# Performance work log

Hardware: AMD Instinct MI355X
Metric: run time of the kernel (lower is better)

## Reference

```python
import jax, jax.numpy as jnp
import numpy as np
import math

TOPK = 13
NC = 80
ALPHA = 1.0
BETA = 6.0
EPS = 1e-9


def _xyxy2wh(b):
    return b[..., 2:4] - b[..., 0:2]


def _bbox_ciou(box1, box2, eps=1e-7):
    # box1: [bs,nmax,1,4] gt, box2: [bs,1,na,4] pred, xyxy. Returns [bs,nmax,na].
    b1x1, b1y1, b1x2, b1y2 = jnp.split(box1, 4, axis=-1)
    b2x1, b2y1, b2x2, b2y2 = jnp.split(box2, 4, axis=-1)
    w1, h1 = b1x2 - b1x1, b1y2 - b1y1 + eps
    w2, h2 = b2x2 - b2x1, b2y2 - b2y1 + eps
    inter = jnp.clip(jnp.minimum(b1x2, b2x2) - jnp.maximum(b1x1, b2x1), 0) * \
            jnp.clip(jnp.minimum(b1y2, b2y2) - jnp.maximum(b1y1, b2y1), 0)
    union = w1 * h1 + w2 * h2 - inter + eps
    iou = inter / union
    cw = jnp.maximum(b1x2, b2x2) - jnp.minimum(b1x1, b2x1)  # enclosing box
    ch = jnp.maximum(b1y2, b2y2) - jnp.minimum(b1y1, b2y1)
    c2 = cw ** 2 + ch ** 2 + eps
    rho2 = ((b2x1 + b2x2 - b1x1 - b1x2) ** 2 + (b2y1 + b2y2 - b1y1 - b1y2) ** 2) / 4.0
    v = (4.0 / math.pi ** 2) * (jnp.arctan(w2 / h2) - jnp.arctan(w1 / h1)) ** 2
    a = jax.lax.stop_gradient(v / (v - iou + (1.0 + eps)))  # torch.no_grad alpha
    return (iou - (rho2 / c2 + v * a))[..., 0]


def tal_forward(pd_scores, pd_bboxes, anc_points, gt_labels, gt_bboxes, mask_gt,
                gt_kkpts, pd_kkpts, sigma, stride_tensor, reg_max):
    bs, na, nc = pd_scores.shape
    nmax = gt_bboxes.shape[1]
    dt = pd_scores.dtype
    mgt = mask_gt[..., 0]  # [bs,nmax]

    # --- select_candidates_in_gts: anchor center strictly inside gt box ---
    lt = gt_bboxes[:, :, None, :2]              # [bs,nmax,1,2]
    rb = gt_bboxes[:, :, None, 2:]
    anc = anc_points[None, None]                # [1,1,na,2]
    deltas = jnp.concatenate([anc - lt, rb - anc], -1)  # [bs,nmax,na,4]
    mask_in_gts = (deltas.min(-1) > EPS).astype(dt)

    # --- my_filter_anchor: anchor max predictable box edge >= gt mean edge ---
    aps_max = stride_tensor[:, 0] * (reg_max - 1) * 2          # [na]
    gt_size = _xyxy2wh(gt_bboxes).mean(-1)                     # [bs,nmax] (w+h)/2
    filt = (aps_max[None, None, :] - gt_size[..., None] >= EPS).astype(dt)
    mask_in_gts = mask_in_gts * filt

    m = mask_in_gts * mask_gt  # [bs,nmax,na] float 0/1 (mask_in_gts * mask_gt)

    # --- get_box_metrics ---
    lbl = gt_labels[..., 0].astype(jnp.int32)                  # [bs,nmax]
    onehot = jax.nn.one_hot(lbl, nc, dtype=dt)
    bbox_scores = jnp.einsum('bnc,bgc->bgn', pd_scores, onehot) * m

    iou = jnp.clip(_bbox_ciou(gt_bboxes[:, :, None, :], pd_bboxes[:, None, :, :]), 0)

    # OKS-style keypoint iou (my_kpt_iou)
    area = (_xyxy2wh(gt_bboxes).prod(-1) * 0.53)[:, :, None, None]   # [bs,nmax,1,1]
    kmask = (gt_kkpts[..., 2] != 0)[:, :, None, :].astype(dt)        # [bs,nmax,1,nk]
    d = (pd_kkpts[:, None, :, :, 0] - gt_kkpts[:, :, None, :, 0]) ** 2 + \
        (pd_kkpts[:, None, :, :, 1] - gt_kkpts[:, :, None, :, 1]) ** 2  # [bs,nmax,na,nk]
    e = d / ((2.0 * sigma) ** 2) / (area + 1e-7) / 2.0
    kpt_iou = (jnp.exp(-e) * kmask).sum(-1) / (kmask.sum(-1) + 1e-7)
    kpt_iou = jnp.clip(kpt_iou, 0)

    overlaps = ((iou + kpt_iou) / 2.0) * m
    align_metric = (bbox_scores ** ALPHA) * (overlaps ** BETA)

    # --- select_topk_candidates ---
    topk_mask = jnp.broadcast_to(mgt[:, :, None] > 0, (bs, nmax, TOPK))
    _, idxs = jax.lax.top_k(align_metric, TOPK)                # [bs,nmax,TOPK]
    idxs = jnp.where(topk_mask, idxs, 0)
    flat = idxs.reshape(bs * nmax, TOPK)
    cnt = jnp.zeros((bs * nmax, na), jnp.int32).at[
        jnp.arange(bs * nmax)[:, None], flat].add(1)
    cnt = cnt.reshape(bs, nmax, na)
    mask_topk = jnp.where(cnt > 1, 0, cnt).astype(dt)          # drop duplicated idx 0

    mask_pos = mask_topk * mask_in_gts * mask_gt

    # --- select_highest_overlaps ---
    fg = mask_pos.sum(-2)                                      # [bs,na]
    multi = fg[:, None, :] > 1
    is_max = jax.nn.one_hot(overlaps.argmax(1), nmax, dtype=dt).transpose(0, 2, 1)
    mask_pos = jnp.where(multi, is_max, mask_pos)
    fg = mask_pos.sum(-2)
    tgi = mask_pos.argmax(-2)                                  # [bs,na] target gt idx

    # --- get_targets ---
    flat_idx = tgi + jnp.arange(bs, dtype=tgi.dtype)[:, None] * nmax
    tlabels = jnp.clip(gt_labels.reshape(-1)[flat_idx], 0)     # [bs,na]
    tbboxes = gt_bboxes.reshape(-1, 4)[flat_idx]               # [bs,na,4]
    tscores = jax.nn.one_hot(tlabels, nc, dtype=dt)
    tscores = jnp.where(fg[..., None] > 0, tscores, 0.0)

    # --- normalize scores by aligned metric ---
    align_metric = align_metric * mask_pos
    pos_align = align_metric.max(-1, keepdims=True)            # [bs,nmax,1]
    pos_ov = (overlaps * mask_pos).max(-1, keepdims=True)
    norm = (align_metric * pos_ov / (pos_align + EPS)).max(-2)[..., None]  # [bs,na,1]
    tscores = tscores * norm
    return tlabels, tbboxes, tscores, fg > 0, tgi


def setup_inputs() -> dict:
    key = jax.random.key(0)
    ks = jax.random.split(key, 10)
    bs, nmax, nc, nk = 16, 64, 80, 1
    pts, strs = [], []
    for s, n in [(8, 80), (16, 40), (32, 20)]:
        g = (jnp.arange(n, dtype=jnp.float32) + 0.5) * s
        yv, xv = jnp.meshgrid(g, g, indexing='ij')
        pts.append(jnp.stack([xv.ravel(), yv.ravel()], -1))
        strs.append(jnp.full((n * n, 1), float(s), jnp.float32))
    anc_points = jnp.concatenate(pts, 0)        # [8400,2]
    stride_tensor = jnp.concatenate(strs, 0)    # [8400,1]
    na = anc_points.shape[0]

    def boxes(k, shape):
        k1, k2 = jax.random.split(k)
        c = jax.random.uniform(k1, shape + (2,), jnp.float32, 60.0, 580.0)
        wh = jax.random.uniform(k2, shape + (2,), jnp.float32, 10.0, 120.0)
        return jnp.concatenate([c - wh / 2, c + wh / 2], -1)

    pd_scores = jax.random.uniform(ks[0], (bs, na, nc), jnp.float32)
    pd_bboxes = boxes(ks[1], (bs, na))
    gt_bboxes = boxes(ks[2], (bs, nmax))
    gt_labels = jax.random.randint(ks[3], (bs, nmax, 1), 0, nc)
    mask_gt = (jax.random.uniform(ks[4], (bs, nmax, 1)) < 0.7).astype(jnp.float32)
    gt_xy = jax.random.uniform(ks[5], (bs, nmax, nk, 2), jnp.float32, 0.0, 640.0)
    gt_v = jax.random.randint(ks[6], (bs, nmax, nk, 1), 0, 3).astype(jnp.float32)
    gt_kkpts = jnp.concatenate([gt_xy, gt_v], -1)
    pd_xy = jax.random.uniform(ks[7], (bs, na, nk, 2), jnp.float32, 0.0, 640.0)
    pd_v = jax.random.uniform(ks[8], (bs, na, nk, 1), jnp.float32)
    pd_kkpts = jnp.concatenate([pd_xy, pd_v], -1)
    sigma = jnp.full((nk,), 0.25, jnp.float32)
    return dict(pd_scores=pd_scores, pd_bboxes=pd_bboxes, anc_points=anc_points,
                gt_labels=gt_labels, gt_bboxes=gt_bboxes, mask_gt=mask_gt,
                gt_kkpts=gt_kkpts, pd_kkpts=pd_kkpts, sigma=sigma,
                stride_tensor=stride_tensor, reg_max=16)


def reference(pd_scores, pd_bboxes, anc_points, gt_labels, gt_bboxes, mask_gt,
              gt_kkpts, pd_kkpts, sigma, stride_tensor, reg_max):
    return tal_forward(pd_scores, pd_bboxes, anc_points, gt_labels, gt_bboxes,
                       mask_gt, gt_kkpts, pd_kkpts, sigma, stride_tensor, reg_max)
```

## Files before the change

kernel.cpp:

```cpp
#include <hip/hip_runtime.h>
#include <math.h>
#include <float.h>
#include <limits.h>

#define TOPK 13
typedef unsigned int u32;
typedef unsigned long long u64;

__device__ __forceinline__ u32 q32f(double x) {
  if (!(x > 0.0)) return 0u;
  float f = (float)x;
  u32 b = __float_as_uint(f);
  return (b >= 0x00800000u) ? b : 0u;
}
__device__ __forceinline__ double val32(u32 b) {
  return (double)__uint_as_float(b);
}

struct MetricQ { u32 amb; u32 ovb; bool m; };

__device__ MetricQ metric_at(
    const float* __restrict__ pd_scores, const float* __restrict__ pd_bboxes,
    const float* __restrict__ anc, const int* __restrict__ gt_labels,
    const float* __restrict__ gt_bboxes, const float* __restrict__ mask_gt,
    const float* __restrict__ gt_kkpts, const float* __restrict__ pd_kkpts,
    const float* __restrict__ sigma, const float* __restrict__ stride_t,
    int reg_max, int b, int g, int a, int nmax, int na, int nc, int nk)
{
#pragma clang fp contract(off)
  MetricQ r; r.amb = 0u; r.ovb = 0u; r.m = false;
  const float* gb = gt_bboxes + (size_t)(b * nmax + g) * 4;
  float gx1 = gb[0], gy1 = gb[1], gx2 = gb[2], gy2 = gb[3];
  float mgt = mask_gt[b * nmax + g];
  float ax = anc[(size_t)a * 2 + 0], ay = anc[(size_t)a * 2 + 1];
  float dmin = fminf(fminf(ax - gx1, ay - gy1), fminf(gx2 - ax, gy2 - ay));
  float aps = (stride_t[a] * (float)(reg_max - 1)) * 2.0f;
  float gw = gx2 - gx1, gh = gy2 - gy1;
  float gsize = (gw + gh) * 0.5f;
  bool mm = ((double)dmin > 1e-9) && ((double)(aps - gsize) >= 1e-9) && (mgt > 0.f);
  r.m = mm;
  if (!mm) return r;

  int lbl = gt_labels[b * nmax + g];
  float score = pd_scores[((size_t)(b * na + a)) * nc + lbl];

  const float* pb = pd_bboxes + ((size_t)(b * na + a)) * 4;
  float px1 = pb[0], py1 = pb[1], px2 = pb[2], py2 = pb[3];
  const float e7 = 1e-7f;
  float w1 = gx2 - gx1, h1 = (gy2 - gy1) + e7;
  float w2 = px2 - px1, h2 = (py2 - py1) + e7;
  float iw = fmaxf(fminf(gx2, px2) - fmaxf(gx1, px1), 0.f);
  float ih = fmaxf(fminf(gy2, py2) - fmaxf(gy1, py1), 0.f);
  float inter = iw * ih;
  float uni = ((w1 * h1 + w2 * h2) - inter) + e7;
  float iou = inter / uni;
  float cw = fmaxf(gx2, px2) - fminf(gx1, px1);
  float ch = fmaxf(gy2, py2) - fminf(gy1, py1);
  float c2 = (cw * cw + ch * ch) + e7;
  float dcx = ((px1 + px2) - gx1) - gx2;
  float dcy = ((py1 + py2) - gy1) - gy2;
  float rho2 = (dcx * dcx + dcy * dcy) / 4.0f;
  float a2 = (float)atan((double)(w2 / h2));
  float a1 = (float)atan((double)(w1 / h1));
  float arc = a2 - a1;
  const float C = (float)(4.0 / (3.14159265358979323846 * 3.14159265358979323846));
  float v = C * (arc * arc);
  const float C1 = (float)(1.0 + 1e-7);
  float al = v / ((v - iou) + C1);
  float ciou = iou - (rho2 / c2 + v * al);
  float iouc = fmaxf(ciou, 0.f);

  float area = (gw * gh) * 0.53f;
  double ksum = 0.0;
  float  kcnt = 0.f;
  for (int k = 0; k < nk; k++) {
    const float* gk = gt_kkpts + ((size_t)(b * nmax + g) * nk + k) * 3;
    const float* pk = pd_kkpts + (((size_t)(b * na + a)) * nk + k) * 3;
    float km = (gk[2] != 0.f) ? 1.f : 0.f;
    float dx = pk[0] - gk[0], dy = pk[1] - gk[1];
    float d  = dx * dx + dy * dy;
    float s2 = 2.f * sigma[k]; s2 = s2 * s2;
    float e1 = d / s2;
    float e2 = e1 / (area + 1e-7f);
    float e  = e2 / 2.0f;
    double s1 = val32(q32f(exp(-(double)e)));
    double term = s1 * (double)km;
    ksum = val32(q32f(ksum + term));
    kcnt = kcnt + km;
  }
  double den = (double)(kcnt + 1e-7f);
  u32 kioub = q32f(ksum / den);
  double kiou = val32(kioub);
  u32 sumb = q32f((double)iouc + kiou);
  u32 ovlb = q32f(val32(sumb) * 0.5);
  double ovl = val32(ovlb);
  u32 p6b = q32f(pow(ovl, 6.0));
  u32 amb = q32f((double)score * val32(p6b));
  r.ovb = ovlb;
  r.amb = amb;
  return r;
}

__global__ void k_zeroi(int* __restrict__ p, long n) {
  long i = (long)blockIdx.x * blockDim.x + threadIdx.x;
  if (i < n) p[i] = 0;
}

#define MAXC 512

__global__ void k_rows(const float* __restrict__ pd_scores, const float* __restrict__ pd_bboxes,
                       const float* __restrict__ anc, const int* __restrict__ gt_labels,
                       const float* __restrict__ gt_bboxes, const float* __restrict__ mask_gt,
                       const float* __restrict__ gt_kkpts, const float* __restrict__ pd_kkpts,
                       const float* __restrict__ sigma, const float* __restrict__ stride_t,
                       const int* __restrict__ reg_max_p,
                       int* __restrict__ cnt, int* __restrict__ gsel,
                       u32* __restrict__ amsel, u32* __restrict__ ovsel,
                       int bs, int nmax, int na, int nc, int nk)
{
  int g = blockIdx.x, b = blockIdx.y;
  if (mask_gt[b * nmax + g] <= 0.f) return;
  int reg_max = reg_max_p[0];
  int tid = threadIdx.x;
  int wave = tid >> 6, lane = tid & 63;

  __shared__ int   s_ncand;
  __shared__ int   s_cand[MAXC];
  __shared__ u32   s_keyv[MAXC];
  __shared__ u32   s_ovv[MAXC];
  __shared__ unsigned short s_ciOf[1024];
  __shared__ u32   s_bitPos[32];
  __shared__ int   s_selA[TOPK];
  __shared__ int   s_selCi[TOPK];

  if (tid == 0) s_ncand = 0;
  if (tid < 32) s_bitPos[tid] = 0u;
  for (int i = tid; i < 1024; i += 256) s_ciOf[i] = 0xFFFF;
  __syncthreads();

  {
    const float* gb = gt_bboxes + (size_t)(b * nmax + g) * 4;
    float gx1 = gb[0], gy1 = gb[1], gx2 = gb[2], gy2 = gb[3];
    float gw = gx2 - gx1, gh = gy2 - gy1;
    float gsize = (gw + gh) * 0.5f;
    const float2* anc2 = (const float2*)anc;
    for (int a = tid; a < na; a += 256) {
      float2 av = anc2[a];
      float dmin = fminf(fminf(av.x - gx1, av.y - gy1), fminf(gx2 - av.x, gy2 - av.y));
      float aps = (stride_t[a] * (float)(reg_max - 1)) * 2.0f;
      bool mm = ((double)dmin > 1e-9) && ((double)(aps - gsize) >= 1e-9);
      if (mm) {
        int ci = atomicAdd(&s_ncand, 1);
        if (ci < MAXC) {
          s_cand[ci] = a;
          if (a < 1024) s_ciOf[a] = (unsigned short)ci;
        }
      }
    }
  }
  __syncthreads();
  int ncand = min(s_ncand, MAXC);

  for (int ci = tid; ci < ncand; ci += 256) {
    int a = s_cand[ci];
    MetricQ mt = metric_at(pd_scores, pd_bboxes, anc, gt_labels, gt_bboxes, mask_gt,
                           gt_kkpts, pd_kkpts, sigma, stride_t, reg_max,
                           b, g, a, nmax, na, nc, nk);
    s_keyv[ci] = mt.amb;
    s_ovv[ci]  = mt.ovb;
    if (mt.amb != 0u && a < 1024) atomicOr(&s_bitPos[a >> 5], 1u << (a & 31));
  }
  __syncthreads();

  if (wave == 0) {
    u64 kk[8];
#pragma unroll
    for (int j = 0; j < 8; j++) {
      int ci = lane + (j << 6);
      u64 v = 0;
      if (ci < ncand) {
        u32 amb = s_keyv[ci];
        if (amb != 0u)
          v = ((u64)amb << 32) | (u64)(u32)(0xFFFFFFFFu - (u32)s_cand[ci]);
      }
      kk[j] = v;
    }
    int np = TOPK;
    for (int k = 0; k < TOPK; k++) {
      u64 best = 0; int bj = 0;
#pragma unroll
      for (int j = 0; j < 8; j++) if (kk[j] > best) { best = kk[j]; bj = j; }
      u64 p = best;
      for (int off = 32; off; off >>= 1) {
        u64 q = __shfl_xor(p, off);
        if (q > p) p = q;
      }
      if ((u32)(p >> 32) == 0u) { np = k; break; }
      if (best == p) {
        s_selA[k]  = (int)(0xFFFFFFFFu - (u32)p);
        s_selCi[k] = lane + (bj << 6);
        kk[bj] = 0;
      }
    }
    if (lane == 0) {
      int a = 0;
      for (int k = np; k < TOPK; k++) {
        while ((s_bitPos[a >> 5] >> (a & 31)) & 1u) a++;
        s_selA[k] = a;
        s_selCi[k] = (s_ciOf[a] == 0xFFFF) ? -1 : (int)s_ciOf[a];
        a++;
      }
    }
  }
  __syncthreads();

  if (tid < TOPK) {
    int ci = s_selCi[tid];
    if (ci >= 0) {
      int a = s_selA[tid];
      int t = b * na + a;
      atomicAdd(&cnt[t], 1);
      gsel[t] = g;
      amsel[t] = s_keyv[ci];
      ovsel[t] = s_ovv[ci];
    }
  }
}

__global__ void k_anchors(const int* __restrict__ gt_labels, const float* __restrict__ gt_bboxes,
                          const int* __restrict__ cnt, const int* __restrict__ gsel,
                          const u32* __restrict__ amsel, const u32* __restrict__ ovsel,
                          u32* __restrict__ pa, u32* __restrict__ po,
                          u32* __restrict__ amfin, float* __restrict__ out,
                          int* __restrict__ mcount, int* __restrict__ mlist,
                          int bs, int nmax, int na, int nc,
                          long tb_off, long fg_off, long tgi_off)
{
  int t = blockIdx.x * blockDim.x + threadIdx.x;
  if (t >= bs * na) return;
  int b = t / na;

  int c = cnt[t];
  if (c > 1) {
    int i = atomicAdd(mcount, 1);
    mlist[i] = t;
    return;
  }
  int tgi = 0; u32 amb = 0u, ovb = 0u; bool fg = false;
  if (c == 1) { tgi = gsel[t]; amb = amsel[t]; ovb = ovsel[t]; fg = true; }

  int lbl = gt_labels[b * nmax + tgi]; if (lbl < 0) lbl = 0;
  out[t] = (float)lbl;
  const float* gb = gt_bboxes + (size_t)(b * nmax + tgi) * 4;
  float* tb = out + tb_off + (long)t * 4;
  tb[0] = gb[0]; tb[1] = gb[1]; tb[2] = gb[2]; tb[3] = gb[3];
  out[fg_off + t] = fg ? 1.0f : 0.0f;
  out[tgi_off + t] = (float)tgi;

  amfin[t] = amb;
  if (fg) {
    int row = b * nmax + tgi;
    atomicMax(&pa[row], amb);
    atomicMax(&po[row], ovb);
  }
}

__global__ void k_multi(const float* __restrict__ pd_scores, const float* __restrict__ pd_bboxes,
                        const float* __restrict__ anc, const int* __restrict__ gt_labels,
                        const float* __restrict__ gt_bboxes, const float* __restrict__ mask_gt,
                        const float* __restrict__ gt_kkpts, const float* __restrict__ pd_kkpts,
                        const float* __restrict__ sigma, const float* __restrict__ stride_t,
                        const int* __restrict__ reg_max_p,
                        const int* __restrict__ mcount, const int* __restrict__ mlist,
                        u32* __restrict__ pa, u32* __restrict__ po,
                        u32* __restrict__ amfin, float* __restrict__ out,
                        int bs, int nmax, int na, int nc, int nk,
                        long tb_off, long fg_off, long tgi_off)
{
  int waveId = (int)((blockIdx.x * blockDim.x + threadIdx.x) >> 6);
  int lane   = threadIdx.x & 63;
  int nwaves = (int)((gridDim.x * blockDim.x) >> 6);
  int reg_max = reg_max_p[0];
  int M = mcount[0];

  for (int i = waveId; i < M; i += nwaves) {
    int t = mlist[i];
    int b = t / na, a = t - b * na;
    u32 ovg = 0u, amg = 0u;
    if (lane < nmax) {
      MetricQ mt = metric_at(pd_scores, pd_bboxes, anc, gt_labels, gt_bboxes, mask_gt,
                             gt_kkpts, pd_kkpts, sigma, stride_t, reg_max,
                             b, lane, a, nmax, na, nc, nk);
      ovg = mt.m ? mt.ovb : 0u;
      amg = mt.m ? mt.amb : 0u;
    }
    u64 p = ((u64)ovg << 32) | (u64)(u32)(0xFFFFFFFFu - (u32)lane);
    for (int off = 32; off; off >>= 1) {
      u64 q = __shfl_xor(p, off);
      if (q > p) p = q;
    }
    int wg = (int)(0xFFFFFFFFu - (u32)(p & 0xFFFFFFFFu));
    if (lane == wg) {
      int lbl = gt_labels[b * nmax + wg]; if (lbl < 0) lbl = 0;
      out[t] = (float)lbl;
      const float* gb = gt_bboxes + (size_t)(b * nmax + wg) * 4;
      float* tb = out + tb_off + (long)t * 4;
      tb[0] = gb[0]; tb[1] = gb[1]; tb[2] = gb[2]; tb[3] = gb[3];
      out[fg_off + t] = 1.0f;
      out[tgi_off + t] = (float)wg;
      amfin[t] = amg;
      int row = b * nmax + wg;
      atomicMax(&pa[row], amg);
      atomicMax(&po[row], ovg);
    }
  }
}

__global__ void k_scores(const u32* __restrict__ pa, const u32* __restrict__ po,
                         const u32* __restrict__ amfin, float* __restrict__ out,
                         int bs, int nmax, int na, int nc, long ts_off, long fg_off, long tgi_off)
{
  __shared__ float s_val[64];
  __shared__ int   s_lbl[64];
  long nba = (long)bs * na;
  long base = (long)blockIdx.x * 64;
  int tid = threadIdx.x;

  if (tid < 64) {
    long t = base + tid;
    float v = 0.f; int lbl = 0;
    if (t < nba && out[fg_off + t] > 0.f) {
      int b = (int)(t / na);
      int tgi = (int)out[tgi_off + t];
      int row = b * nmax + tgi;
      u32 rb = q32f(val32(po[row]) / (val32(pa[row]) + (double)1e-9f));
      u32 nb = q32f(val32(amfin[t]) * val32(rb));
      v = __uint_as_float(nb);
      lbl = (int)out[t];
    }
    s_val[tid] = v; s_lbl[tid] = lbl;
  }
  __syncthreads();

  int nA = (int)min((long)64, nba - base);
  if (nA <= 0) return;

  if ((nc & 3) == 0) {
    int nc4 = nc >> 2;
    float4* dst = (float4*)(out + ts_off + base * nc);
    int total = nA * nc4;
    for (int q = tid; q < total; q += 256) {
      int aIdx = q / nc4, c4 = (q - aIdx * nc4) << 2;
      float v = s_val[aIdx]; int lbl = s_lbl[aIdx];
      float4 o = make_float4(0.f, 0.f, 0.f, 0.f);
      int d = lbl - c4;
      if (d >= 0 && d < 4) ((float*)&o)[d] = v;
      dst[q] = o;
    }
  } else {
    float* dst = out + ts_off + base * nc;
    int total = nA * nc;
    for (int q = tid; q < total; q += 256) {
      int aIdx = q / nc, c = q - aIdx * nc;
      dst[q] = (c == s_lbl[aIdx]) ? s_val[aIdx] : 0.f;
    }
  }
}

extern "C" void kernel_launch(void* const* d_in, const int* in_sizes, int n_in,
                              void* d_out, int out_size, void* d_ws, size_t ws_size,
                              hipStream_t stream) {
  const float* pd_scores = (const float*)d_in[0];
  const float* pd_bboxes = (const float*)d_in[1];
  const float* anc       = (const float*)d_in[2];
  const int*   gt_labels = (const int*)  d_in[3];
  const float* gt_bboxes = (const float*)d_in[4];
  const float* mask_gt   = (const float*)d_in[5];
  const float* gt_kkpts  = (const float*)d_in[6];
  const float* pd_kkpts  = (const float*)d_in[7];
  const float* sigma     = (const float*)d_in[8];
  const float* stride_t  = (const float*)d_in[9];
  const int*   reg_max_p = (const int*)  d_in[10];

  int na   = in_sizes[2] / 2;
  int bs   = in_sizes[1] / (na * 4);
  int nc   = in_sizes[0] / (bs * na);
  int nmax = in_sizes[3] / bs;
  int nk   = in_sizes[8];

  long nba = (long)bs * na;
  int  R   = bs * nmax;

  int* cnt    = (int*)d_ws;
  u32* pa     = (u32*)(cnt + nba);
  u32* po     = pa + R;
  int* mcount = (int*)(po + R);
  int* gsel   = mcount + 64;
  u32* amsel  = (u32*)(gsel + nba);
  u32* ovsel  = amsel + nba;
  u32* amfin  = ovsel + nba;
  int* mlist  = (int*)(amfin + nba);

  float* out = (float*)d_out;
  long tb_off  = nba;
  long ts_off  = nba * 5;
  long fg_off  = ts_off + nba * nc;
  long tgi_off = fg_off + nba;

  long nz = nba + 2L * R + 64;
  k_zeroi<<<(int)((nz + 255) / 256), 256, 0, stream>>>(cnt, nz);

  dim3 grows(nmax, bs);
  k_rows<<<grows, 256, 0, stream>>>(pd_scores, pd_bboxes, anc, gt_labels, gt_bboxes,
                                    mask_gt, gt_kkpts, pd_kkpts, sigma, stride_t,
                                    reg_max_p, cnt, gsel, amsel, ovsel,
                                    bs, nmax, na, nc, nk);

  int nthr = (int)((nba + 255) / 256);
  k_anchors<<<nthr, 256, 0, stream>>>(gt_labels, gt_bboxes, cnt, gsel, amsel, ovsel,
                                      pa, po, amfin, out, mcount, mlist,
                                      bs, nmax, na, nc, tb_off, fg_off, tgi_off);

  k_multi<<<256, 256, 0, stream>>>(pd_scores, pd_bboxes, anc, gt_labels, gt_bboxes,
                                   mask_gt, gt_kkpts, pd_kkpts, sigma, stride_t,
                                   reg_max_p, mcount, mlist, pa, po, amfin, out,
                                   bs, nmax, na, nc, nk, tb_off, fg_off, tgi_off);

  int nblk_s = (int)((nba + 63) / 64);
  k_scores<<<nblk_s, 256, 0, stream>>>(pa, po, amfin, out, bs, nmax, na, nc,
                                       ts_off, fg_off, tgi_off);
}
```

Baseline: 163.1 us.

## Fuse five kernel launches into one cooperative persistent kernel with grid syncs

```diff
diff --git a/kernel.cpp b/kernel.cpp
--- a/kernel.cpp
+++ b/kernel.cpp
@@ -1,7 +1,10 @@
 #include <hip/hip_runtime.h>
+#include <hip/hip_cooperative_groups.h>
 #include <math.h>
 #include <float.h>
 #include <limits.h>
+
+namespace cg = cooperative_groups;
 
 #define TOPK 13
 typedef unsigned int u32;
@@ -101,28 +104,28 @@
   return r;
 }
 
-__global__ void k_zeroi(int* __restrict__ p, long n) {
-  long i = (long)blockIdx.x * blockDim.x + threadIdx.x;
-  if (i < n) p[i] = 0;
-}
-
 #define MAXC 512
 
-__global__ void k_rows(const float* __restrict__ pd_scores, const float* __restrict__ pd_bboxes,
-                       const float* __restrict__ anc, const int* __restrict__ gt_labels,
-                       const float* __restrict__ gt_bboxes, const float* __restrict__ mask_gt,
-                       const float* __restrict__ gt_kkpts, const float* __restrict__ pd_kkpts,
-                       const float* __restrict__ sigma, const float* __restrict__ stride_t,
-                       const int* __restrict__ reg_max_p,
-                       int* __restrict__ cnt, int* __restrict__ gsel,
-                       u32* __restrict__ amsel, u32* __restrict__ ovsel,
-                       int bs, int nmax, int na, int nc, int nk)
-{
-  int g = blockIdx.x, b = blockIdx.y;
-  if (mask_gt[b * nmax + g] <= 0.f) return;
-  int reg_max = reg_max_p[0];
-  int tid = threadIdx.x;
-  int wave = tid >> 6, lane = tid & 63;
+struct Args {
+  const float* pd_scores; const float* pd_bboxes; const float* anc;
+  const int*   gt_labels; const float* gt_bboxes; const float* mask_gt;
+  const float* gt_kkpts;  const float* pd_kkpts;  const float* sigma;
+  const float* stride_t;  const int*   reg_max_p;
+  int* cnt; u32* pa; u32* po; int* mcount; int* gsel;
+  u32* amsel; u32* ovsel; u32* amfin; int* mlist;
+  float* out;
+  int bs, nmax, na, nc, nk;
+  long tb_off, ts_off, fg_off, tgi_off;
+  long nba; int R;
+};
+
+__global__ void __launch_bounds__(256, 2) k_fused(Args A) {
+  cg::grid_group grid = cg::this_grid();
+  const int tid  = threadIdx.x;
+  const int wave = tid >> 6, lane = tid & 63;
+  const long gtid  = (long)blockIdx.x * blockDim.x + tid;
+  const long gsize = (long)gridDim.x * blockDim.x;
+  const int reg_max = A.reg_max_p[0];
 
   __shared__ int   s_ncand;
   __shared__ int   s_cand[MAXC];
@@ -132,237 +135,226 @@
   __shared__ u32   s_bitPos[32];
   __shared__ int   s_selA[TOPK];
   __shared__ int   s_selCi[TOPK];
-
-  if (tid == 0) s_ncand = 0;
-  if (tid < 32) s_bitPos[tid] = 0u;
-  for (int i = tid; i < 1024; i += 256) s_ciOf[i] = 0xFFFF;
-  __syncthreads();
+  __shared__ float s_val[64];
+  __shared__ int   s_lbl[64];
 
   {
-    const float* gb = gt_bboxes + (size_t)(b * nmax + g) * 4;
-    float gx1 = gb[0], gy1 = gb[1], gx2 = gb[2], gy2 = gb[3];
-    float gw = gx2 - gx1, gh = gy2 - gy1;
-    float gsize = (gw + gh) * 0.5f;
-    const float2* anc2 = (const float2*)anc;
-    for (int a = tid; a < na; a += 256) {
-      float2 av = anc2[a];
-      float dmin = fminf(fminf(av.x - gx1, av.y - gy1), fminf(gx2 - av.x, gy2 - av.y));
-      float aps = (stride_t[a] * (float)(reg_max - 1)) * 2.0f;
-      bool mm = ((double)dmin > 1e-9) && ((double)(aps - gsize) >= 1e-9);
-      if (mm) {
-        int ci = atomicAdd(&s_ncand, 1);
-        if (ci < MAXC) {
-          s_cand[ci] = a;
-          if (a < 1024) s_ciOf[a] = (unsigned short)ci;
-        }
-      }
-    }
-  }
-  __syncthreads();
-  int ncand = min(s_ncand, MAXC);
-
-  for (int ci = tid; ci < ncand; ci += 256) {
-    int a = s_cand[ci];
-    MetricQ mt = metric_at(pd_scores, pd_bboxes, anc, gt_labels, gt_bboxes, mask_gt,
-                           gt_kkpts, pd_kkpts, sigma, stride_t, reg_max,
-                           b, g, a, nmax, na, nc, nk);
-    s_keyv[ci] = mt.amb;
-    s_ovv[ci]  = mt.ovb;
-    if (mt.amb != 0u && a < 1024) atomicOr(&s_bitPos[a >> 5], 1u << (a & 31));
-  }
-  __syncthreads();
-
-  if (wave == 0) {
-    u64 kk[8];
+    long nz = A.nba + 2L * A.R + 64;
+    int* zp = A.cnt;
+    for (long i = gtid; i < nz; i += gsize) zp[i] = 0;
+  }
+  grid.sync();
+
+  for (int row = blockIdx.x; row < A.bs * A.nmax; row += gridDim.x) {
+    if (A.mask_gt[row] <= 0.f) continue;
+    int b = row / A.nmax, g = row - b * A.nmax;
+
+    if (tid == 0) s_ncand = 0;
+    if (tid < 32) s_bitPos[tid] = 0u;
+    for (int i = tid; i < 1024; i += 256) s_ciOf[i] = 0xFFFF;
+    __syncthreads();
+
+    {
+      const float* gb = A.gt_bboxes + (size_t)row * 4;
+      float gx1 = gb[0], gy1 = gb[1], gx2 = gb[2], gy2 = gb[3];
+      float gw = gx2 - gx1, gh = gy2 - gy1;
+      float gsizev = (gw + gh) * 0.5f;
+      const float2* anc2 = (const float2*)A.anc;
+      for (int a = tid; a < A.na; a += 256) {
+        float2 av = anc2[a];
+        float dmin = fminf(fminf(av.x - gx1, av.y - gy1), fminf(gx2 - av.x, gy2 - av.y));
+        float aps = (A.stride_t[a] * (float)(reg_max - 1)) * 2.0f;
+        bool mm = ((double)dmin > 1e-9) && ((double)(aps - gsizev) >= 1e-9);
+        if (mm) {
+          int ci = atomicAdd(&s_ncand, 1);
+          if (ci < MAXC) {
+            s_cand[ci] = a;
+            if (a < 1024) s_ciOf[a] = (unsigned short)ci;
+          }
+        }
+      }
+    }
+    __syncthreads();
+    int ncand = min(s_ncand, MAXC);
+
+    for (int ci = tid; ci < ncand; ci += 256) {
+      int a = s_cand[ci];
+      MetricQ mt = metric_at(A.pd_scores, A.pd_bboxes, A.anc, A.gt_labels, A.gt_bboxes,
+                             A.mask_gt, A.gt_kkpts, A.pd_kkpts, A.sigma, A.stride_t,
+                             reg_max, b, g, a, A.nmax, A.na, A.nc, A.nk);
+      s_keyv[ci] = mt.amb;
+      s_ovv[ci]  = mt.ovb;
+      if (mt.amb != 0u && a < 1024) atomicOr(&s_bitPos[a >> 5], 1u << (a & 31));
+    }
+    __syncthreads();
+
+    if (wave == 0) {
+      u64 kk[8];
 #pragma unroll
-    for (int j = 0; j < 8; j++) {
-      int ci = lane + (j << 6);
-      u64 v = 0;
-      if (ci < ncand) {
-        u32 amb = s_keyv[ci];
-        if (amb != 0u)
-          v = ((u64)amb << 32) | (u64)(u32)(0xFFFFFFFFu - (u32)s_cand[ci]);
-      }
-      kk[j] = v;
-    }
-    int np = TOPK;
-    for (int k = 0; k < TOPK; k++) {
-      u64 best = 0; int bj = 0;
+      for (int j = 0; j < 8; j++) {
+        int ci = lane + (j << 6);
+        u64 v = 0;
+        if (ci < ncand) {
+          u32 amb = s_keyv[ci];
+          if (amb != 0u)
+            v = ((u64)amb << 32) | (u64)(u32)(0xFFFFFFFFu - (u32)s_cand[ci]);
+        }
+        kk[j] = v;
+      }
+      int np = TOPK;
+      for (int k = 0; k < TOPK; k++) {
+        u64 best = 0; int bj = 0;
 #pragma unroll
-      for (int j = 0; j < 8; j++) if (kk[j] > best) { best = kk[j]; bj = j; }
-      u64 p = best;
+        for (int j = 0; j < 8; j++) if (kk[j] > best) { best = kk[j]; bj = j; }
+        u64 p = best;
+        for (int off = 32; off; off >>= 1) {
+          u64 q = __shfl_xor(p, off);
+          if (q > p) p = q;
+        }
+        if ((u32)(p >> 32) == 0u) { np = k; break; }
+        if (best == p) {
+          s_selA[k]  = (int)(0xFFFFFFFFu - (u32)p);
+          s_selCi[k] = lane + (bj << 6);
+          kk[bj] = 0;
+        }
+      }
+      if (lane == 0) {
+        int a = 0;
+        for (int k = np; k < TOPK; k++) {
+          while ((s_bitPos[a >> 5] >> (a & 31)) & 1u) a++;
+          s_selA[k] = a;
+          s_selCi[k] = (s_ciOf[a] == 0xFFFF) ? -1 : (int)s_ciOf[a];
+          a++;
+        }
+      }
+    }
+    __syncthreads();
+
+    if (tid < TOPK) {
+      int ci = s_selCi[tid];
+      if (ci >= 0) {
+        int a = s_selA[tid];
+        int t = b * A.na + a;
+        atomicAdd(&A.cnt[t], 1);
+        A.gsel[t] = g;
+        A.amsel[t] = s_keyv[ci];
+        A.ovsel[t] = s_ovv[ci];
+      }
+    }
+    __syncthreads();
+  }
+  grid.sync();
+
+  for (long t = gtid; t < A.nba; t += gsize) {
+    int b = (int)(t / A.na);
+    int c = A.cnt[t];
+    if (c > 1) {
+      int i = atomicAdd(A.mcount, 1);
+      A.mlist[i] = (int)t;
+      continue;
+    }
+    int tgi = 0; u32 amb = 0u, ovb = 0u; bool fg = false;
+    if (c == 1) { tgi = A.gsel[t]; amb = A.amsel[t]; ovb = A.ovsel[t]; fg = true; }
+
+    int lbl = A.gt_labels[b * A.nmax + tgi]; if (lbl < 0) lbl = 0;
+    A.out[t] = (float)lbl;
+    const float* gb = A.gt_bboxes + (size_t)(b * A.nmax + tgi) * 4;
+    float* tb = A.out + A.tb_off + t * 4;
+    tb[0] = gb[0]; tb[1] = gb[1]; tb[2] = gb[2]; tb[3] = gb[3];
+    A.out[A.fg_off + t] = fg ? 1.0f : 0.0f;
+    A.out[A.tgi_off + t] = (float)tgi;
+
+    A.amfin[t] = amb;
+    if (fg) {
+      int rw = b * A.nmax + tgi;
+      atomicMax(&A.pa[rw], amb);
+      atomicMax(&A.po[rw], ovb);
+    }
+  }
+  grid.sync();
+
+  {
+    long waveId = gtid >> 6;
+    long nwaves = gsize >> 6;
+    int M = A.mcount[0];
+    for (long i = waveId; i < M; i += nwaves) {
+      int t = A.mlist[i];
+      int b = t / A.na, a = t - b * A.na;
+      u32 ovg = 0u, amg = 0u;
+      if (lane < A.nmax) {
+        MetricQ mt = metric_at(A.pd_scores, A.pd_bboxes, A.anc, A.gt_labels, A.gt_bboxes,
+                               A.mask_gt, A.gt_kkpts, A.pd_kkpts, A.sigma, A.stride_t,
+                               reg_max, b, lane, a, A.nmax, A.na, A.nc, A.nk);
+        ovg = mt.m ? mt.ovb : 0u;
+        amg = mt.m ? mt.amb : 0u;
+      }
+      u64 p = ((u64)ovg << 32) | (u64)(u32)(0xFFFFFFFFu - (u32)lane);
       for (int off = 32; off; off >>= 1) {
         u64 q = __shfl_xor(p, off);
         if (q > p) p = q;
       }
-      if ((u32)(p >> 32) == 0u) { np = k; break; }
-      if (best == p) {
-        s_selA[k]  = (int)(0xFFFFFFFFu - (u32)p);
-        s_selCi[k] = lane + (bj << 6);
-        kk[bj] = 0;
-      }
-    }
-    if (lane == 0) {
-      int a = 0;
-      for (int k = np; k < TOPK; k++) {
-        while ((s_bitPos[a >> 5] >> (a & 31)) & 1u) a++;
-        s_selA[k] = a;
-        s_selCi[k] = (s_ciOf[a] == 0xFFFF) ? -1 : (int)s_ciOf[a];
-        a++;
-      }
-    }
-  }
-  __syncthreads();
-
-  if (tid < TOPK) {
-    int ci = s_selCi[tid];
-    if (ci >= 0) {
-      int a = s_selA[tid];
-      int t = b * na + a;
-      atomicAdd(&cnt[t], 1);
-      gsel[t] = g;
-      amsel[t] = s_keyv[ci];
-      ovsel[t] = s_ovv[ci];
-    }
-  }
-}
-
-__global__ void k_anchors(const int* __restrict__ gt_labels, const float* __restrict__ gt_bboxes,
-                          const int* __restrict__ cnt, const int* __restrict__ gsel,
-                          const u32* __restrict__ amsel, const u32* __restrict__ ovsel,
-                          u32* __restrict__ pa, u32* __restrict__ po,
-                          u32* __restrict__ amfin, float* __restrict__ out,
-                          int* __restrict__ mcount, int* __restrict__ mlist,
-                          int bs, int nmax, int na, int nc,
-                          long tb_off, long fg_off, long tgi_off)
-{
-  int t = blockIdx.x * blockDim.x + threadIdx.x;
-  if (t >= bs * na) return;
-  int b = t / na;
-
-  int c = cnt[t];
-  if (c > 1) {
-    int i = atomicAdd(mcount, 1);
-    mlist[i] = t;
-    return;
-  }
-  int tgi = 0; u32 amb = 0u, ovb = 0u; bool fg = false;
-  if (c == 1) { tgi = gsel[t]; amb = amsel[t]; ovb = ovsel[t]; fg = true; }
-
-  int lbl = gt_labels[b * nmax + tgi]; if (lbl < 0) lbl = 0;
-  out[t] = (float)lbl;
-  const float* gb = gt_bboxes + (size_t)(b * nmax + tgi) * 4;
-  float* tb = out + tb_off + (long)t * 4;
-  tb[0] = gb[0]; tb[1] = gb[1]; tb[2] = gb[2]; tb[3] = gb[3];
-  out[fg_off + t] = fg ? 1.0f : 0.0f;
-  out[tgi_off + t] = (float)tgi;
-
-  amfin[t] = amb;
-  if (fg) {
-    int row = b * nmax + tgi;
-    atomicMax(&pa[row], amb);
-    atomicMax(&po[row], ovb);
-  }
-}
-
-__global__ void k_multi(const float* __restrict__ pd_scores, const float* __restrict__ pd_bboxes,
-                        const float* __restrict__ anc, const int* __restrict__ gt_labels,
-                        const float* __restrict__ gt_bboxes, const float* __restrict__ mask_gt,
-                        const float* __restrict__ gt_kkpts, const float* __restrict__ pd_kkpts,
-                        const float* __restrict__ sigma, const float* __restrict__ stride_t,
-                        const int* __restrict__ reg_max_p,
-                        const int* __restrict__ mcount, const int* __restrict__ mlist,
-                        u32* __restrict__ pa, u32* __restrict__ po,
-                        u32* __restrict__ amfin, float* __restrict__ out,
-                        int bs, int nmax, int na, int nc, int nk,
-                        long tb_off, long fg_off, long tgi_off)
-{
-  int waveId = (int)((blockIdx.x * blockDim.x + threadIdx.x) >> 6);
-  int lane   = threadIdx.x & 63;
-  int nwaves = (int)((gridDim.x * blockDim.x) >> 6);
-  int reg_max = reg_max_p[0];
-  int M = mcount[0];
-
-  for (int i = waveId; i < M; i += nwaves) {
-    int t = mlist[i];
-    int b = t / na, a = t - b * na;
-    u32 ovg = 0u, amg = 0u;
-    if (lane < nmax) {
-      MetricQ mt = metric_at(pd_scores, pd_bboxes, anc, gt_labels, gt_bboxes, mask_gt,
-                             gt_kkpts, pd_kkpts, sigma, stride_t, reg_max,
-                             b, lane, a, nmax, na, nc, nk);
-      ovg = mt.m ? mt.ovb : 0u;
-      amg = mt.m ? mt.amb : 0u;
-    }
-    u64 p = ((u64)ovg << 32) | (u64)(u32)(0xFFFFFFFFu - (u32)lane);
-    for (int off = 32; off; off >>= 1) {
-      u64 q = __shfl_xor(p, off);
-      if (q > p) p = q;
-    }
-    int wg = (int)(0xFFFFFFFFu - (u32)(p & 0xFFFFFFFFu));
-    if (lane == wg) {
-      int lbl = gt_labels[b * nmax + wg]; if (lbl < 0) lbl = 0;
-      out[t] = (float)lbl;
-      const float* gb = gt_bboxes + (size_t)(b * nmax + wg) * 4;
-      float* tb = out + tb_off + (long)t * 4;
-      tb[0] = gb[0]; tb[1] = gb[1]; tb[2] = gb[2]; tb[3] = gb[3];
-      out[fg_off + t] = 1.0f;
-      out[tgi_off + t] = (float)wg;
-      amfin[t] = amg;
-      int row = b * nmax + wg;
-      atomicMax(&pa[row], amg);
-      atomicMax(&po[row], ovg);
-    }
-  }
-}
-
-__global__ void k_scores(const u32* __restrict__ pa, const u32* __restrict__ po,
-                         const u32* __restrict__ amfin, float* __restrict__ out,
-                         int bs, int nmax, int na, int nc, long ts_off, long fg_off, long tgi_off)
-{
-  __shared__ float s_val[64];
-  __shared__ int   s_lbl[64];
-  long nba = (long)bs * na;
-  long base = (long)blockIdx.x * 64;
-  int tid = threadIdx.x;
-
-  if (tid < 64) {
-    long t = base + tid;
-    float v = 0.f; int lbl = 0;
-    if (t < nba && out[fg_off + t] > 0.f) {
-      int b = (int)(t / na);
-      int tgi = (int)out[tgi_off + t];
-      int row = b * nmax + tgi;
-      u32 rb = q32f(val32(po[row]) / (val32(pa[row]) + (double)1e-9f));
-      u32 nb = q32f(val32(amfin[t]) * val32(rb));
-      v = __uint_as_float(nb);
-      lbl = (int)out[t];
-    }
-    s_val[tid] = v; s_lbl[tid] = lbl;
-  }
-  __syncthreads();
-
-  int nA = (int)min((long)64, nba - base);
-  if (nA <= 0) return;
-
-  if ((nc & 3) == 0) {
-    int nc4 = nc >> 2;
-    float4* dst = (float4*)(out + ts_off + base * nc);
-    int total = nA * nc4;
-    for (int q = tid; q < total; q += 256) {
-      int aIdx = q / nc4, c4 = (q - aIdx * nc4) << 2;
-      float v = s_val[aIdx]; int lbl = s_lbl[aIdx];
-      float4 o = make_float4(0.f, 0.f, 0.f, 0.f);
-      int d = lbl - c4;
-      if (d >= 0 && d < 4) ((float*)&o)[d] = v;
-      dst[q] = o;
-    }
-  } else {
-    float* dst = out + ts_off + base * nc;
-    int total = nA * nc;
-    for (int q = tid; q < total; q += 256) {
-      int aIdx = q / nc, c = q - aIdx * nc;
-      dst[q] = (c == s_lbl[aIdx]) ? s_val[aIdx] : 0.f;
+      int wg = (int)(0xFFFFFFFFu - (u32)(p & 0xFFFFFFFFu));
+      if (lane == wg) {
+        int lbl = A.gt_labels[b * A.nmax + wg]; if (lbl < 0) lbl = 0;
+        A.out[t] = (float)lbl;
+        const float* gb = A.gt_bboxes + (size_t)(b * A.nmax + wg) * 4;
+        float* tb = A.out + A.tb_off + (long)t * 4;
+        tb[0] = gb[0]; tb[1] = gb[1]; tb[2] = gb[2]; tb[3] = gb[3];
+        A.out[A.fg_off + t] = 1.0f;
+        A.out[A.tgi_off + t] = (float)wg;
+        A.amfin[t] = amg;
+        int rw = b * A.nmax + wg;
+        atomicMax(&A.pa[rw], amg);
+        atomicMax(&A.po[rw], ovg);
+      }
+    }
+  }
+  grid.sync();
+
+  {
+    long ntiles = (A.nba + 63) / 64;
+    for (long tile = blockIdx.x; tile < ntiles; tile += gridDim.x) {
+      long base = tile * 64;
+      if (tid < 64) {
+        long t = base + tid;
+        float v = 0.f; int lbl = 0;
+        if (t < A.nba && A.out[A.fg_off + t] > 0.f) {
+          int b = (int)(t / A.na);
+          int tgi = (int)A.out[A.tgi_off + t];
+          int rw = b * A.nmax + tgi;
+          u32 rb = q32f(val32(A.po[rw]) / (val32(A.pa[rw]) + (double)1e-9f));
+          u32 nb = q32f(val32(A.amfin[t]) * val32(rb));
+          v = __uint_as_float(nb);
+          lbl = (int)A.out[t];
+        }
+        s_val[tid] = v; s_lbl[tid] = lbl;
+      }
+      __syncthreads();
+
+      int nA = (int)min((long)64, A.nba - base);
+      if (nA > 0) {
+        if ((A.nc & 3) == 0) {
+          int nc4 = A.nc >> 2;
+          float4* dst = (float4*)(A.out + A.ts_off + base * A.nc);
+          int total = nA * nc4;
+          for (int q = tid; q < total; q += 256) {
+            int aIdx = q / nc4, c4 = (q - aIdx * nc4) << 2;
+            float v = s_val[aIdx]; int lbl = s_lbl[aIdx];
+            float4 o = make_float4(0.f, 0.f, 0.f, 0.f);
+            int d = lbl - c4;
+            if (d >= 0 && d < 4) ((float*)&o)[d] = v;
+            dst[q] = o;
+          }
+        } else {
+          float* dst = A.out + A.ts_off + base * A.nc;
+          int total = nA * A.nc;
+          for (int q = tid; q < total; q += 256) {
+            int aIdx = q / A.nc, c = q - aIdx * A.nc;
+            dst[q] = (c == s_lbl[aIdx]) ? s_val[aIdx] : 0.f;
+          }
+        }
+      }
+      __syncthreads();
     }
   }
 }
@@ -402,31 +394,35 @@
   int* mlist  = (int*)(amfin + nba);
 
   float* out = (float*)d_out;
-  long tb_off  = nba;
-  long ts_off  = nba * 5;
-  long fg_off  = ts_off + nba * nc;
-  long tgi_off = fg_off + nba;
-
-  long nz = nba + 2L * R + 64;
-  k_zeroi<<<(int)((nz + 255) / 256), 256, 0, stream>>>(cnt, nz);
-
-  dim3 grows(nmax, bs);
-  k_rows<<<grows, 256, 0, stream>>>(pd_scores, pd_bboxes, anc, gt_labels, gt_bboxes,
-                                    mask_gt, gt_kkpts, pd_kkpts, sigma, stride_t,
-                                    reg_max_p, cnt, gsel, amsel, ovsel,
-                                    bs, nmax, na, nc, nk);
-
-  int nthr = (int)((nba + 255) / 256);
-  k_anchors<<<nthr, 256, 0, stream>>>(gt_labels, gt_bboxes, cnt, gsel, amsel, ovsel,
-                                      pa, po, amfin, out, mcount, mlist,
-                                      bs, nmax, na, nc, tb_off, fg_off, tgi_off);
-
-  k_multi<<<256, 256, 0, stream>>>(pd_scores, pd_bboxes, anc, gt_labels, gt_bboxes,
-                                   mask_gt, gt_kkpts, pd_kkpts, sigma, stride_t,
-                                   reg_max_p, mcount, mlist, pa, po, amfin, out,
-                                   bs, nmax, na, nc, nk, tb_off, fg_off, tgi_off);
-
-  int nblk_s = (int)((nba + 63) / 64);
-  k_scores<<<nblk_s, 256, 0, stream>>>(pa, po, amfin, out, bs, nmax, na, nc,
-                                       ts_off, fg_off, tgi_off);
+
+  Args A;
+  A.pd_scores = pd_scores; A.pd_bboxes = pd_bboxes; A.anc = anc;
+  A.gt_labels = gt_labels; A.gt_bboxes = gt_bboxes; A.mask_gt = mask_gt;
+  A.gt_kkpts = gt_kkpts;   A.pd_kkpts = pd_kkpts;   A.sigma = sigma;
+  A.stride_t = stride_t;   A.reg_max_p = reg_max_p;
+  A.cnt = cnt; A.pa = pa; A.po = po; A.mcount = mcount; A.gsel = gsel;
+  A.amsel = amsel; A.ovsel = ovsel; A.amfin = amfin; A.mlist = mlist;
+  A.out = out;
+  A.bs = bs; A.nmax = nmax; A.na = na; A.nc = nc; A.nk = nk;
+  A.tb_off  = nba;
+  A.ts_off  = nba * 5;
+  A.fg_off  = A.ts_off + nba * nc;
+  A.tgi_off = A.fg_off + nba;
+  A.nba = nba; A.R = R;
+
+  static int nblk = 0;
+  if (nblk == 0) {
+    int nCU = 256, maxB = 0;
+    hipDeviceProp_t prop;
+    if (hipGetDeviceProperties(&prop, 0) == hipSuccess && prop.multiProcessorCount > 0)
+      nCU = prop.multiProcessorCount;
+    if (hipOccupancyMaxActiveBlocksPerMultiprocessor(&maxB, (const void*)k_fused, 256, 0) != hipSuccess || maxB < 1)
+      maxB = 1;
+    long cap = (long)maxB * nCU;
+    nblk = (int)(cap < 512 ? cap : 512);
+    if (nblk < 1) nblk = 1;
+  }
+
+  void* params[] = { (void*)&A };
+  hipLaunchCooperativeKernel((const void*)k_fused, dim3(nblk), dim3(256), params, 0u, stream);
 }
```

New measurement: 340.2 us. +108.5%, slower.

## Fuse anchor assignment and multi-GT resolution, drop zeroing kernel via per-row selection lists

Applied to the files above, without the earlier changes.

```diff
diff --git a/kernel.cpp b/kernel.cpp
--- a/kernel.cpp
+++ b/kernel.cpp
@@ -101,12 +101,8 @@
   return r;
 }
 
-__global__ void k_zeroi(int* __restrict__ p, long n) {
-  long i = (long)blockIdx.x * blockDim.x + threadIdx.x;
-  if (i < n) p[i] = 0;
-}
-
 #define MAXC 512
+#define NMAX_MAX 64
 
 __global__ void k_rows(const float* __restrict__ pd_scores, const float* __restrict__ pd_bboxes,
                        const float* __restrict__ anc, const int* __restrict__ gt_labels,
@@ -114,15 +110,25 @@
                        const float* __restrict__ gt_kkpts, const float* __restrict__ pd_kkpts,
                        const float* __restrict__ sigma, const float* __restrict__ stride_t,
                        const int* __restrict__ reg_max_p,
-                       int* __restrict__ cnt, int* __restrict__ gsel,
-                       u32* __restrict__ amsel, u32* __restrict__ ovsel,
+                       int* __restrict__ sel_a, u32* __restrict__ sel_am, u32* __restrict__ sel_ov,
+                       u32* __restrict__ pa, u32* __restrict__ po,
                        int bs, int nmax, int na, int nc, int nk)
 {
   int g = blockIdx.x, b = blockIdx.y;
-  if (mask_gt[b * nmax + g] <= 0.f) return;
-  int reg_max = reg_max_p[0];
+  int row = b * nmax + g;
   int tid = threadIdx.x;
   int wave = tid >> 6, lane = tid & 63;
+
+  if (tid == 0) { pa[row] = 0u; po[row] = 0u; }
+  if (mask_gt[row] <= 0.f) {
+    if (tid < TOPK) {
+      sel_a [row * TOPK + tid] = -1;
+      sel_am[row * TOPK + tid] = 0u;
+      sel_ov[row * TOPK + tid] = 0u;
+    }
+    return;
+  }
+  int reg_max = reg_max_p[0];
 
   __shared__ int   s_ncand;
   __shared__ int   s_cand[MAXC];
@@ -139,16 +145,16 @@
   __syncthreads();
 
   {
-    const float* gb = gt_bboxes + (size_t)(b * nmax + g) * 4;
+    const float* gb = gt_bboxes + (size_t)row * 4;
     float gx1 = gb[0], gy1 = gb[1], gx2 = gb[2], gy2 = gb[3];
     float gw = gx2 - gx1, gh = gy2 - gy1;
-    float gsize = (gw + gh) * 0.5f;
+    float gsizev = (gw + gh) * 0.5f;
     const float2* anc2 = (const float2*)anc;
     for (int a = tid; a < na; a += 256) {
       float2 av = anc2[a];
       float dmin = fminf(fminf(av.x - gx1, av.y - gy1), fminf(gx2 - av.x, gy2 - av.y));
       float aps = (stride_t[a] * (float)(reg_max - 1)) * 2.0f;
-      bool mm = ((double)dmin > 1e-9) && ((double)(aps - gsize) >= 1e-9);
+      bool mm = ((double)dmin > 1e-9) && ((double)(aps - gsizev) >= 1e-9);
       if (mm) {
         int ci = atomicAdd(&s_ncand, 1);
         if (ci < MAXC) {
@@ -216,81 +222,95 @@
 
   if (tid < TOPK) {
     int ci = s_selCi[tid];
-    if (ci >= 0) {
-      int a = s_selA[tid];
-      int t = b * na + a;
-      atomicAdd(&cnt[t], 1);
-      gsel[t] = g;
-      amsel[t] = s_keyv[ci];
-      ovsel[t] = s_ovv[ci];
-    }
-  }
-}
-
-__global__ void k_anchors(const int* __restrict__ gt_labels, const float* __restrict__ gt_bboxes,
-                          const int* __restrict__ cnt, const int* __restrict__ gsel,
-                          const u32* __restrict__ amsel, const u32* __restrict__ ovsel,
-                          u32* __restrict__ pa, u32* __restrict__ po,
-                          u32* __restrict__ amfin, float* __restrict__ out,
-                          int* __restrict__ mcount, int* __restrict__ mlist,
-                          int bs, int nmax, int na, int nc,
-                          long tb_off, long fg_off, long tgi_off)
+    bool ok = (ci >= 0);
+    sel_a [row * TOPK + tid] = ok ? s_selA[tid] : -1;
+    sel_am[row * TOPK + tid] = ok ? s_keyv[ci] : 0u;
+    sel_ov[row * TOPK + tid] = ok ? s_ovv[ci] : 0u;
+  }
+}
+
+__global__ void __launch_bounds__(256) k_anchmul(
+    const float* __restrict__ pd_scores, const float* __restrict__ pd_bboxes,
+    const float* __restrict__ anc, const int* __restrict__ gt_labels,
+    const float* __restrict__ gt_bboxes, const float* __restrict__ mask_gt,
+    const float* __restrict__ gt_kkpts, const float* __restrict__ pd_kkpts,
+    const float* __restrict__ sigma, const float* __restrict__ stride_t,
+    const int* __restrict__ reg_max_p,
+    const int* __restrict__ sel_a, const u32* __restrict__ sel_am, const u32* __restrict__ sel_ov,
+    u32* __restrict__ pa, u32* __restrict__ po,
+    u32* __restrict__ amfin, float* __restrict__ out,
+    int bs, int nmax, int na, int nc, int nk,
+    long tb_off, long fg_off, long tgi_off)
 {
-  int t = blockIdx.x * blockDim.x + threadIdx.x;
-  if (t >= bs * na) return;
-  int b = t / na;
-
-  int c = cnt[t];
-  if (c > 1) {
-    int i = atomicAdd(mcount, 1);
-    mlist[i] = t;
-    return;
-  }
-  int tgi = 0; u32 amb = 0u, ovb = 0u; bool fg = false;
-  if (c == 1) { tgi = gsel[t]; amb = amsel[t]; ovb = ovsel[t]; fg = true; }
-
-  int lbl = gt_labels[b * nmax + tgi]; if (lbl < 0) lbl = 0;
-  out[t] = (float)lbl;
-  const float* gb = gt_bboxes + (size_t)(b * nmax + tgi) * 4;
-  float* tb = out + tb_off + (long)t * 4;
-  tb[0] = gb[0]; tb[1] = gb[1]; tb[2] = gb[2]; tb[3] = gb[3];
-  out[fg_off + t] = fg ? 1.0f : 0.0f;
-  out[tgi_off + t] = (float)tgi;
-
-  amfin[t] = amb;
-  if (fg) {
-    int row = b * nmax + tgi;
-    atomicMax(&pa[row], amb);
-    atomicMax(&po[row], ovb);
-  }
-}
-
-__global__ void k_multi(const float* __restrict__ pd_scores, const float* __restrict__ pd_bboxes,
-                        const float* __restrict__ anc, const int* __restrict__ gt_labels,
-                        const float* __restrict__ gt_bboxes, const float* __restrict__ mask_gt,
-                        const float* __restrict__ gt_kkpts, const float* __restrict__ pd_kkpts,
-                        const float* __restrict__ sigma, const float* __restrict__ stride_t,
-                        const int* __restrict__ reg_max_p,
-                        const int* __restrict__ mcount, const int* __restrict__ mlist,
-                        u32* __restrict__ pa, u32* __restrict__ po,
-                        u32* __restrict__ amfin, float* __restrict__ out,
-                        int bs, int nmax, int na, int nc, int nk,
-                        long tb_off, long fg_off, long tgi_off)
-{
-  int waveId = (int)((blockIdx.x * blockDim.x + threadIdx.x) >> 6);
-  int lane   = threadIdx.x & 63;
-  int nwaves = (int)((gridDim.x * blockDim.x) >> 6);
+  int b = blockIdx.y;
+  int a = blockIdx.x * 256 + threadIdx.x;
+  int tid = threadIdx.x;
+  int lane = tid & 63;
   int reg_max = reg_max_p[0];
-  int M = mcount[0];
-
-  for (int i = waveId; i < M; i += nwaves) {
-    int t = mlist[i];
-    int b = t / na, a = t - b * na;
+
+  __shared__ int sh_a [NMAX_MAX * TOPK];
+  __shared__ u32 sh_am[NMAX_MAX * TOPK];
+  __shared__ u32 sh_ov[NMAX_MAX * TOPK];
+  __shared__ int sh_qn;
+  __shared__ int sh_q[256];
+
+  if (tid == 0) sh_qn = 0;
+  const int nsel = nmax * TOPK;
+  {
+    const size_t base = (size_t)b * nsel;
+    for (int i = tid; i < nsel; i += 256) {
+      sh_a [i] = sel_a [base + i];
+      sh_am[i] = sel_am[base + i];
+      sh_ov[i] = sel_ov[base + i];
+    }
+  }
+  __syncthreads();
+
+  bool valid = (a < na);
+  int c = 0, mi = 0;
+  if (valid) {
+    for (int i = 0; i < nsel; i++) {
+      bool m = (sh_a[i] == a);
+      c  += m ? 1 : 0;
+      mi  = m ? i : mi;
+    }
+  }
+
+  if (valid) {
+    long t = (long)b * na + a;
+    if (c > 1) {
+      int qi = atomicAdd(&sh_qn, 1);
+      sh_q[qi] = a;
+    } else {
+      int tgi = 0; u32 amb = 0u, ovb = 0u; bool fg = false;
+      if (c == 1) { tgi = mi / TOPK; amb = sh_am[mi]; ovb = sh_ov[mi]; fg = true; }
+      int lbl = gt_labels[b * nmax + tgi]; if (lbl < 0) lbl = 0;
+      out[t] = (float)lbl;
+      const float* gb = gt_bboxes + (size_t)(b * nmax + tgi) * 4;
+      float* tb = out + tb_off + t * 4;
+      tb[0] = gb[0]; tb[1] = gb[1]; tb[2] = gb[2]; tb[3] = gb[3];
+      out[fg_off + t] = fg ? 1.0f : 0.0f;
+      out[tgi_off + t] = (float)tgi;
+      amfin[t] = amb;
+      if (fg) {
+        int rw = b * nmax + tgi;
+        atomicMax(&pa[rw], amb);
+        atomicMax(&po[rw], ovb);
+      }
+    }
+  }
+  __syncthreads();
+
+  int qn = sh_qn;
+  int wave = tid >> 6;
+  for (int i = wave; i < qn; i += 4) {
+    int aa = sh_q[i];
+    long t = (long)b * na + aa;
     u32 ovg = 0u, amg = 0u;
     if (lane < nmax) {
       MetricQ mt = metric_at(pd_scores, pd_bboxes, anc, gt_labels, gt_bboxes, mask_gt,
                              gt_kkpts, pd_kkpts, sigma, stride_t, reg_max,
-                             b, lane, a, nmax, na, nc, nk);
+                             b, lane, aa, nmax, na, nc, nk);
       ovg = mt.m ? mt.ovb : 0u;
       amg = mt.m ? mt.amb : 0u;
     }
@@ -304,14 +324,14 @@
       int lbl = gt_labels[b * nmax + wg]; if (lbl < 0) lbl = 0;
       out[t] = (float)lbl;
       const float* gb = gt_bboxes + (size_t)(b * nmax + wg) * 4;
-      float* tb = out + tb_off + (long)t * 4;
+      float* tb = out + tb_off + t * 4;
       tb[0] = gb[0]; tb[1] = gb[1]; tb[2] = gb[2]; tb[3] = gb[3];
       out[fg_off + t] = 1.0f;
       out[tgi_off + t] = (float)wg;
       amfin[t] = amg;
-      int row = b * nmax + wg;
-      atomicMax(&pa[row], amg);
-      atomicMax(&po[row], ovg);
+      int rw = b * nmax + wg;
+      atomicMax(&pa[rw], amg);
+      atomicMax(&po[rw], ovg);
     }
   }
 }
@@ -391,15 +411,12 @@
   long nba = (long)bs * na;
   int  R   = bs * nmax;
 
-  int* cnt    = (int*)d_ws;
-  u32* pa     = (u32*)(cnt + nba);
+  int* sel_a  = (int*)d_ws;
+  u32* sel_am = (u32*)(sel_a + (long)R * TOPK);
+  u32* sel_ov = sel_am + (long)R * TOPK;
+  u32* pa     = sel_ov + (long)R * TOPK;
   u32* po     = pa + R;
-  int* mcount = (int*)(po + R);
-  int* gsel   = mcount + 64;
-  u32* amsel  = (u32*)(gsel + nba);
-  u32* ovsel  = amsel + nba;
-  u32* amfin  = ovsel + nba;
-  int* mlist  = (int*)(amfin + nba);
+  u32* amfin  = po + R;
 
   float* out = (float*)d_out;
   long tb_off  = nba;
@@ -407,24 +424,18 @@
   long fg_off  = ts_off + nba * nc;
   long tgi_off = fg_off + nba;
 
-  long nz = nba + 2L * R + 64;
-  k_zeroi<<<(int)((nz + 255) / 256), 256, 0, stream>>>(cnt, nz);
-
   dim3 grows(nmax, bs);
   k_rows<<<grows, 256, 0, stream>>>(pd_scores, pd_bboxes, anc, gt_labels, gt_bboxes,
                                     mask_gt, gt_kkpts, pd_kkpts, sigma, stride_t,
-                                    reg_max_p, cnt, gsel, amsel, ovsel,
+                                    reg_max_p, sel_a, sel_am, sel_ov, pa, po,
                                     bs, nmax, na, nc, nk);
 
-  int nthr = (int)((nba + 255) / 256);
-  k_anchors<<<nthr, 256, 0, stream>>>(gt_labels, gt_bboxes, cnt, gsel, amsel, ovsel,
-                                      pa, po, amfin, out, mcount, mlist,
-                                      bs, nmax, na, nc, tb_off, fg_off, tgi_off);
-
-  k_multi<<<256, 256, 0, stream>>>(pd_scores, pd_bboxes, anc, gt_labels, gt_bboxes,
-                                   mask_gt, gt_kkpts, pd_kkpts, sigma, stride_t,
-                                   reg_max_p, mcount, mlist, pa, po, amfin, out,
-                                   bs, nmax, na, nc, nk, tb_off, fg_off, tgi_off);
+  dim3 ganch((na + 255) / 256, bs);
+  k_anchmul<<<ganch, 256, 0, stream>>>(pd_scores, pd_bboxes, anc, gt_labels, gt_bboxes,
+                                       mask_gt, gt_kkpts, pd_kkpts, sigma, stride_t,
+                                       reg_max_p, sel_a, sel_am, sel_ov, pa, po,
+                                       amfin, out, bs, nmax, na, nc, nk,
+                                       tb_off, fg_off, tgi_off);
 
   int nblk_s = (int)((nba + 63) / 64);
   k_scores<<<nblk_s, 256, 0, stream>>>(pa, po, amfin, out, bs, nmax, na, nc,
```

Result: slower. 184.3 us (+13.0%).
